# Kernel optimization log

Hardware: AMD Instinct MI355X
Metric: run time of the kernel (lower is better)

Reference implementation:

```python
import jax, jax.numpy as jnp
import numpy as np

B, S, D, H, DH = 2, 2048, 256, 8, 32
INNER = H * DH


def setup_inputs() -> dict:
    key = jax.random.key(0)
    ks = jax.random.split(key, 8)
    x = jax.random.normal(ks[0], (B, S, D), dtype=jnp.float32)
    mask = jax.random.randint(ks[1], (B, S), 0, 2) > 0  # bool, ~half valid
    attn_bias = jax.random.normal(ks[2], (B, H, S, S), dtype=jnp.float32) * 0.1
    Wq = jax.random.normal(ks[3], (D, INNER), dtype=jnp.float32) * 0.02
    Wkv = jax.random.normal(ks[4], (D, 2 * INNER), dtype=jnp.float32) * 0.02
    Wo = jax.random.normal(ks[5], (INNER, D), dtype=jnp.float32) * 0.02
    bo = jnp.zeros((D,), dtype=jnp.float32)
    Wg = jax.random.normal(ks[6], (D, INNER), dtype=jnp.float32) * 0.02
    bg = jnp.ones((INNER,), dtype=jnp.float32)  # torch init: gating bias = 1.0
    return {"x": x, "mask": mask, "attn_bias": attn_bias, "Wq": Wq,
            "Wkv": Wkv, "Wo": Wo, "bo": bo, "Wg": Wg, "bg": bg}


def reference(x, mask, attn_bias, Wq, Wkv, Wo, bo, Wg, bg):
    scale = DH ** -0.5
    b, s, _ = x.shape
    # q,k,v projections; '... i (h d) -> ... h i d'
    q = (x @ Wq).reshape(b, s, H, DH).swapaxes(1, 2)            # [b,h,s,d]
    kv = x @ Wkv
    k, v = jnp.split(kv, 2, axis=-1)
    k = k.reshape(b, s, H, DH).swapaxes(1, 2)                   # [b,h,s,d]
    v = v.reshape(b, s, H, DH).swapaxes(1, 2)                   # [b,h,s,d]
    # scores with additive bias and boolean masking
    dots = jnp.einsum('bhid,bhjd->bhij', q * scale, k) + attn_bias
    amask = mask[:, None, :, None] & mask[:, None, None, :]     # [b,1,i,j]
    neg = -jnp.finfo(dots.dtype).max
    dots = jnp.where(amask, dots, neg)
    attn = jax.nn.softmax(dots, axis=-1)                        # dropout p=0 (eval)
    out = jnp.einsum('bhij,bhjd->bhid', attn, v)
    out = out.swapaxes(1, 2).reshape(b, s, INNER)               # '... h i d -> ... i (h d)'
    gates = jax.nn.sigmoid(x @ Wg + bg)
    out = out * gates
    return out @ Wo + bo
```

## Files before the change

kernel.cpp:

```cpp
#include <hip/hip_runtime.h>
#include <float.h>

typedef unsigned short u16;
typedef __attribute__((ext_vector_type(8))) short bf16x8;
typedef __attribute__((ext_vector_type(4))) float f32x4;

#define LOG2E 1.4426950408889634f
#define B_ 2
#define S_ 2048
#define D_ 256
#define H_ 8
#define DH_ 32
#define M_ 4096

__device__ __forceinline__ void gload_lds16(const void* g, void* l) {
  __builtin_amdgcn_global_load_lds(
      (const __attribute__((address_space(1))) unsigned int*)g,
      (__attribute__((address_space(3))) unsigned int*)l, 16, 0, 0);
}

__device__ __forceinline__ u16 f2bf(float f) {
  unsigned u = __float_as_uint(f);
  unsigned r = (u + 0x7FFFu + ((u >> 16) & 1u)) >> 16;
  return (u16)r;
}

__global__ __launch_bounds__(256) void conv_x(const float* __restrict__ x,
                                              u16* __restrict__ xb) {
  int i = (blockIdx.x * 256 + threadIdx.x) * 4;
  float4 v = *(const float4*)(x + i);
  ushort4 o;
  o.x = f2bf(v.x); o.y = f2bf(v.y); o.z = f2bf(v.z); o.w = f2bf(v.w);
  *(ushort4*)(xb + i) = o;
}

__global__ __launch_bounds__(256) void prep_w(const float* __restrict__ Wq,
                                              const float* __restrict__ Wkv,
                                              const float* __restrict__ Wo,
                                              const float* __restrict__ Wg,
                                              u16* __restrict__ wt,
                                              u16* __restrict__ wot) {
  int t = blockIdx.x * 256 + threadIdx.x;
  const float scale = 0.17677669529663687f;
  if (t < 65536) {
    int k = t >> 8, n = t & 255;
    wt[(size_t)n * 256 + k] = f2bf(Wq[t] * scale);
  } else if (t < 196608) {
    int s = t - 65536;
    int k = s >> 9, c = s & 511;
    int n = (c < 256) ? (256 + c) : (512 + (c - 256));
    wt[(size_t)n * 256 + k] = f2bf(Wkv[s]);
  } else if (t < 262144) {
    int s = t - 196608;
    int k = s >> 8, n = s & 255;
    wt[(size_t)(768 + n) * 256 + k] = f2bf(Wg[s]);
  } else {
    int s = t - 262144;
    int k = s >> 8, n = s & 255;
    wot[(size_t)n * 256 + k] = f2bf(Wo[s]);
  }
}

__global__ __launch_bounds__(256) void gemm_proj(
    const u16* __restrict__ xb, const u16* __restrict__ wt,
    const float* __restrict__ bg, u16* __restrict__ qs, u16* __restrict__ kb,
    u16* __restrict__ vt, float* __restrict__ gates) {
  __shared__ u16 lA[128 * 32];
  __shared__ u16 lB[128 * 32];
  const int tid = threadIdx.x, l = tid & 63, w = tid >> 6;
  const int m0 = blockIdx.x * 128, n0 = blockIdx.y * 128;
  const int wm = w >> 1, wn = w & 1;
  f32x4 acc[4][4];
#pragma unroll
  for (int i = 0; i < 4; ++i)
#pragma unroll
    for (int j = 0; j < 4; ++j) acc[i][j] = (f32x4){0.f, 0.f, 0.f, 0.f};

  for (int ks = 0; ks < 8; ++ks) {
#pragma unroll
    for (int i = 0; i < 2; ++i) {
      int slot = i * 256 + tid;
      int row = slot >> 2, sk = slot & 3;
      int sw = sk ^ ((row >> 1) & 3);
      gload_lds16(xb + (size_t)(m0 + row) * 256 + ks * 32 + sw * 8,
                  (char*)lA + slot * 16);
    }
#pragma unroll
    for (int i = 0; i < 2; ++i) {
      int slot = i * 256 + tid;
      int row = slot >> 2, sk = slot & 3;
      int sw = sk ^ ((row >> 1) & 3);
      gload_lds16(wt + (size_t)(n0 + row) * 256 + ks * 32 + sw * 8,
                  (char*)lB + slot * 16);
    }
    __syncthreads();
    bf16x8 af[4], bfr[4];
#pragma unroll
    for (int mi = 0; mi < 4; ++mi) {
      int row = wm * 64 + mi * 16 + (l & 15);
      int koff = ((l >> 4) << 4) ^ (((row >> 1) & 3) << 4);
      af[mi] = *(const bf16x8*)((const char*)lA + row * 64 + koff);
    }
#pragma unroll
    for (int ni = 0; ni < 4; ++ni) {
      int row = wn * 64 + ni * 16 + (l & 15);
      int koff = ((l >> 4) << 4) ^ (((row >> 1) & 3) << 4);
      bfr[ni] = *(const bf16x8*)((const char*)lB + row * 64 + koff);
    }
#pragma unroll
    for (int mi = 0; mi < 4; ++mi)
#pragma unroll
      for (int ni = 0; ni < 4; ++ni)
        acc[mi][ni] = __builtin_amdgcn_mfma_f32_16x16x32_bf16(
            af[mi], bfr[ni], acc[mi][ni], 0, 0, 0);
    __syncthreads();
  }
  const int region = n0 >> 8;
#pragma unroll
  for (int mi = 0; mi < 4; ++mi)
#pragma unroll
    for (int ni = 0; ni < 4; ++ni) {
      int row = m0 + wm * 64 + mi * 16 + ((l >> 4) << 2);
      int col = n0 + wn * 64 + ni * 16 + (l & 15);
      int c = col & 255;
#pragma unroll
      for (int r = 0; r < 4; ++r) {
        float v = acc[mi][ni][r];
        int rr = row + r;
        int bq = rr >> 11, s = rr & 2047;
        if (region == 0) {
          int h = c >> 5, dh = c & 31;
          qs[((((size_t)bq * 8 + h) * 2048 + s) << 5) + dh] = f2bf(v);
        } else if (region == 1) {
          int h = c >> 5, dh = c & 31;
          kb[((((size_t)bq * 8 + h) * 2048 + s) << 5) + dh] = f2bf(v);
        } else if (region == 2) {
          int h = c >> 5, dh = c & 31;
          vt[((((size_t)bq * 8 + h) * 32 + dh) << 11) + s] = f2bf(v);
        } else {
          float g = 1.f / (1.f + expf(-(v + bg[c])));
          gates[(size_t)rr * 256 + c] = g;
        }
      }
    }
}

__global__ __launch_bounds__(256) void attn_fwd(
    const u16* __restrict__ qs, const u16* __restrict__ kb,
    const u16* __restrict__ vt, const float* __restrict__ bias,
    const int* __restrict__ mask, const float* __restrict__ gates,
    u16* __restrict__ ao) {
  __shared__ u16 lK[64 * 32];
  __shared__ u16 lV[32 * 64];
  __shared__ u16 lP[4][16 * 64];
  const int tid = threadIdx.x, l = tid & 63, w = tid >> 6;
  const int qt = blockIdx.x, h = blockIdx.y, b = blockIdx.z;
  const int q0 = qt * 64;
  const size_t bh = (size_t)b * H_ + h;

  const int qrow = q0 + w * 16 + (l & 15);
  bf16x8 qf = *(const bf16x8*)(qs + ((bh * S_ + qrow) << 5) + ((l >> 4) << 3));

  int rowr[4], mi_[4];
  float m_i[4], l_i[4];
  const float* biasrow[4];
  f32x4 acc_o[2];
  acc_o[0] = (f32x4){0.f, 0.f, 0.f, 0.f};
  acc_o[1] = (f32x4){0.f, 0.f, 0.f, 0.f};
#pragma unroll
  for (int r = 0; r < 4; ++r) {
    rowr[r] = q0 + w * 16 + ((l >> 4) << 2) + r;
    mi_[r] = mask[b * S_ + rowr[r]];
    m_i[r] = -FLT_MAX;
    l_i[r] = 0.f;
    biasrow[r] = bias + (bh * S_ + rowr[r]) * (size_t)S_;
  }

  for (int jc = 0; jc < 32; ++jc) {
    const int j0 = jc * 64;
    {
      int row = tid >> 2, sk = tid & 3;
      int sw = sk ^ ((row >> 1) & 3);
      gload_lds16(kb + ((bh * S_ + j0 + row) << 5) + sw * 8,
                  (char*)lK + tid * 16);
    }
    {
      int dh = tid >> 3, sk = tid & 7;
      int sw = sk ^ (dh & 7);
      gload_lds16(vt + ((bh * 32 + dh) << 11) + j0 + sw * 8,
                  (char*)lV + tid * 16);
    }
    __syncthreads();

    f32x4 sc[4];
#pragma unroll
    for (int cg = 0; cg < 4; ++cg) {
      int j = j0 + cg * 16 + (l & 15);
      int mj = mask[b * S_ + j];
      f32x4 ci;
#pragma unroll
      for (int r = 0; r < 4; ++r) {
        float bv = biasrow[r][j];
        ci[r] = (mi_[r] && mj) ? bv : -FLT_MAX;
      }
      int krow = cg * 16 + (l & 15);
      int koff = ((l >> 4) << 4) ^ (((krow >> 1) & 3) << 4);
      bf16x8 kf = *(const bf16x8*)((const char*)lK + krow * 64 + koff);
      sc[cg] = __builtin_amdgcn_mfma_f32_16x16x32_bf16(qf, kf, ci, 0, 0, 0);
    }

    float corr[4];
#pragma unroll
    for (int r = 0; r < 4; ++r) {
      float v0 = fmaxf(fmaxf(sc[0][r], sc[1][r]), fmaxf(sc[2][r], sc[3][r]));
#pragma unroll
      for (int off = 1; off < 16; off <<= 1) v0 = fmaxf(v0, __shfl_xor(v0, off));
      float mn = fmaxf(m_i[r], v0);
      corr[r] = exp2f((m_i[r] - mn) * LOG2E);
      m_i[r] = mn;
    }
    float rs[4] = {0.f, 0.f, 0.f, 0.f};
#pragma unroll
    for (int cg = 0; cg < 4; ++cg) {
#pragma unroll
      for (int r = 0; r < 4; ++r) {
        float p = exp2f((sc[cg][r] - m_i[r]) * LOG2E);
        rs[r] += p;
        int prow = ((l >> 4) << 2) + r;
        int col = cg * 16 + (l & 15);
        *(u16*)((char*)lP[w] + prow * 128 + ((col * 2) ^ ((prow & 7) << 4))) =
            f2bf(p);
      }
    }
#pragma unroll
    for (int r = 0; r < 4; ++r) {
      float s = rs[r];
#pragma unroll
      for (int off = 1; off < 16; off <<= 1) s += __shfl_xor(s, off);
      l_i[r] = l_i[r] * corr[r] + s;
    }
#pragma unroll
    for (int g = 0; g < 2; ++g)
#pragma unroll
      for (int r = 0; r < 4; ++r) acc_o[g][r] *= corr[r];

#pragma unroll
    for (int kp = 0; kp < 2; ++kp) {
      int prow = l & 15;
      int koff = (((l >> 4) << 4) + kp * 64) ^ ((prow & 7) << 4);
      bf16x8 pf = *(const bf16x8*)((const char*)lP[w] + prow * 128 + koff);
#pragma unroll
      for (int g = 0; g < 2; ++g) {
        int vrow = g * 16 + (l & 15);
        int vkoff = (((l >> 4) << 4) + kp * 64) ^ ((vrow & 7) << 4);
        bf16x8 vf = *(const bf16x8*)((const char*)lV + vrow * 128 + vkoff);
        acc_o[g] = __builtin_amdgcn_mfma_f32_16x16x32_bf16(pf, vf, acc_o[g], 0, 0, 0);
      }
    }
    __syncthreads();
  }

#pragma unroll
  for (int g = 0; g < 2; ++g)
#pragma unroll
    for (int r = 0; r < 4; ++r) {
      int rr = rowr[r];
      int dh = g * 16 + (l & 15);
      float gate = gates[(size_t)(b * S_ + rr) * 256 + h * 32 + dh];
      float o = acc_o[g][r] / l_i[r] * gate;
      ao[(size_t)(b * S_ + rr) * 256 + h * 32 + dh] = f2bf(o);
    }
}

__global__ __launch_bounds__(256) void gemm_out(const u16* __restrict__ ao,
                                                const u16* __restrict__ wot,
                                                const float* __restrict__ bo,
                                                float* __restrict__ out) {
  __shared__ u16 lA[128 * 32];
  __shared__ u16 lB[128 * 32];
  const int tid = threadIdx.x, l = tid & 63, w = tid >> 6;
  const int m0 = blockIdx.x * 128, n0 = blockIdx.y * 128;
  const int wm = w >> 1, wn = w & 1;
  f32x4 acc[4][4];
#pragma unroll
  for (int i = 0; i < 4; ++i)
#pragma unroll
    for (int j = 0; j < 4; ++j) acc[i][j] = (f32x4){0.f, 0.f, 0.f, 0.f};

  for (int ks = 0; ks < 8; ++ks) {
#pragma unroll
    for (int i = 0; i < 2; ++i) {
      int slot = i * 256 + tid;
      int row = slot >> 2, sk = slot & 3;
      int sw = sk ^ ((row >> 1) & 3);
      gload_lds16(ao + (size_t)(m0 + row) * 256 + ks * 32 + sw * 8,
                  (char*)lA + slot * 16);
    }
#pragma unroll
    for (int i = 0; i < 2; ++i) {
      int slot = i * 256 + tid;
      int row = slot >> 2, sk = slot & 3;
      int sw = sk ^ ((row >> 1) & 3);
      gload_lds16(wot + (size_t)(n0 + row) * 256 + ks * 32 + sw * 8,
                  (char*)lB + slot * 16);
    }
    __syncthreads();
    bf16x8 af[4], bfr[4];
#pragma unroll
    for (int mi = 0; mi < 4; ++mi) {
      int row = wm * 64 + mi * 16 + (l & 15);
      int koff = ((l >> 4) << 4) ^ (((row >> 1) & 3) << 4);
      af[mi] = *(const bf16x8*)((const char*)lA + row * 64 + koff);
    }
#pragma unroll
    for (int ni = 0; ni < 4; ++ni) {
      int row = wn * 64 + ni * 16 + (l & 15);
      int koff = ((l >> 4) << 4) ^ (((row >> 1) & 3) << 4);
      bfr[ni] = *(const bf16x8*)((const char*)lB + row * 64 + koff);
    }
#pragma unroll
    for (int mi = 0; mi < 4; ++mi)
#pragma unroll
      for (int ni = 0; ni < 4; ++ni)
        acc[mi][ni] = __builtin_amdgcn_mfma_f32_16x16x32_bf16(
            af[mi], bfr[ni], acc[mi][ni], 0, 0, 0);
    __syncthreads();
  }
#pragma unroll
  for (int mi = 0; mi < 4; ++mi)
#pragma unroll
    for (int ni = 0; ni < 4; ++ni) {
      int row = m0 + wm * 64 + mi * 16 + ((l >> 4) << 2);
      int col = n0 + wn * 64 + ni * 16 + (l & 15);
#pragma unroll
      for (int r = 0; r < 4; ++r)
        out[(size_t)(row + r) * 256 + col] = acc[mi][ni][r] + bo[col];
    }
}

extern "C" void kernel_launch(void* const* d_in, const int* in_sizes, int n_in,
                              void* d_out, int out_size, void* d_ws,
                              size_t ws_size, hipStream_t stream) {
  const float* x   = (const float*)d_in[0];
  const int* mask  = (const int*)d_in[1];
  const float* bias = (const float*)d_in[2];
  const float* Wq  = (const float*)d_in[3];
  const float* Wkv = (const float*)d_in[4];
  const float* Wo  = (const float*)d_in[5];
  const float* bo  = (const float*)d_in[6];
  const float* Wg  = (const float*)d_in[7];
  const float* bg  = (const float*)d_in[8];

  char* ws = (char*)d_ws;
  u16* xb      = (u16*)(ws);
  u16* wt      = (u16*)(ws + 2097152);
  u16* wot     = (u16*)(ws + 2621440);
  u16* qs      = (u16*)(ws + 2752512);
  u16* kb      = (u16*)(ws + 4849664);
  u16* vt      = (u16*)(ws + 6946816);
  float* gates = (float*)(ws + 9043968);
  u16* ao      = (u16*)(ws + 13238272);
  float* out   = (float*)d_out;

  conv_x<<<dim3(1024), dim3(256), 0, stream>>>(x, xb);
  prep_w<<<dim3(1280), dim3(256), 0, stream>>>(Wq, Wkv, Wo, Wg, wt, wot);
  gemm_proj<<<dim3(32, 8), dim3(256), 0, stream>>>(xb, wt, bg, qs, kb, vt, gates);
  attn_fwd<<<dim3(32, 8, 2), dim3(256), 0, stream>>>(qs, kb, vt, bias, mask, gates, ao);
  gemm_out<<<dim3(32, 2), dim3(256), 0, stream>>>(ao, wot, bo, out);
}
```

Measured before the change: 430.4 us.

## Double-buffer K/V/bias tiles in attention and projection GEMM; bit-pack key mask

Both gemm_proj and attn_fwd now use double-buffered LDS with async global-to-LDS loads of the next tile issued before computing the current one, synchronised with explicit vmcnt waits and barriers. In attention, the attn_bias tile is also staged through LDS instead of being read as scattered global loads per lane. The key mask is precomputed into per-column bitmasks by a new tiny kernel, so each iteration uses a register shift instead of a global load. This costs more LDS (32KB bias buffers), which may reduce occupancy, plus an extra kernel launch.

```diff
diff --git a/kernel.cpp b/kernel.cpp
--- a/kernel.cpp
+++ b/kernel.cpp
@@ -61,12 +61,22 @@
   }
 }
 
+__global__ __launch_bounds__(64) void pack_mask(const int* __restrict__ mask,
+                                                unsigned* __restrict__ cmT) {
+  int b = blockIdx.x, c = threadIdx.x;
+  unsigned wd = 0;
+#pragma unroll
+  for (int jc = 0; jc < 32; ++jc)
+    wd |= (unsigned)(mask[b * 2048 + jc * 64 + c] & 1) << jc;
+  cmT[b * 64 + c] = wd;
+}
+
 __global__ __launch_bounds__(256) void gemm_proj(
     const u16* __restrict__ xb, const u16* __restrict__ wt,
     const float* __restrict__ bg, u16* __restrict__ qs, u16* __restrict__ kb,
     u16* __restrict__ vt, float* __restrict__ gates) {
-  __shared__ u16 lA[128 * 32];
-  __shared__ u16 lB[128 * 32];
+  __shared__ u16 lA[2][128 * 32];
+  __shared__ u16 lB[2][128 * 32];
   const int tid = threadIdx.x, l = tid & 63, w = tid >> 6;
   const int m0 = blockIdx.x * 128, n0 = blockIdx.y * 128;
   const int wm = w >> 1, wn = w & 1;
@@ -76,14 +86,14 @@
 #pragma unroll
     for (int j = 0; j < 4; ++j) acc[i][j] = (f32x4){0.f, 0.f, 0.f, 0.f};
 
-  for (int ks = 0; ks < 8; ++ks) {
+  auto stage = [&](int ks, int p) {
 #pragma unroll
     for (int i = 0; i < 2; ++i) {
       int slot = i * 256 + tid;
       int row = slot >> 2, sk = slot & 3;
       int sw = sk ^ ((row >> 1) & 3);
       gload_lds16(xb + (size_t)(m0 + row) * 256 + ks * 32 + sw * 8,
-                  (char*)lA + slot * 16);
+                  (char*)lA[p] + slot * 16);
     }
 #pragma unroll
     for (int i = 0; i < 2; ++i) {
@@ -91,21 +101,36 @@
       int row = slot >> 2, sk = slot & 3;
       int sw = sk ^ ((row >> 1) & 3);
       gload_lds16(wt + (size_t)(n0 + row) * 256 + ks * 32 + sw * 8,
-                  (char*)lB + slot * 16);
-    }
-    __syncthreads();
+                  (char*)lB[p] + slot * 16);
+    }
+  };
+
+  stage(0, 0);
+  asm volatile("s_waitcnt vmcnt(0)" ::: "memory");
+  __builtin_amdgcn_s_barrier();
+
+  for (int ks = 0; ks < 8; ++ks) {
+    const int cur = ks & 1;
+    if (ks < 7) {
+      stage(ks + 1, cur ^ 1);
+      asm volatile("s_waitcnt vmcnt(4)" ::: "memory");
+    } else {
+      asm volatile("s_waitcnt vmcnt(0)" ::: "memory");
+    }
+    __builtin_amdgcn_s_barrier();
+
     bf16x8 af[4], bfr[4];
 #pragma unroll
     for (int mi = 0; mi < 4; ++mi) {
       int row = wm * 64 + mi * 16 + (l & 15);
       int koff = ((l >> 4) << 4) ^ (((row >> 1) & 3) << 4);
-      af[mi] = *(const bf16x8*)((const char*)lA + row * 64 + koff);
+      af[mi] = *(const bf16x8*)((const char*)lA[cur] + row * 64 + koff);
     }
 #pragma unroll
     for (int ni = 0; ni < 4; ++ni) {
       int row = wn * 64 + ni * 16 + (l & 15);
       int koff = ((l >> 4) << 4) ^ (((row >> 1) & 3) << 4);
-      bfr[ni] = *(const bf16x8*)((const char*)lB + row * 64 + koff);
+      bfr[ni] = *(const bf16x8*)((const char*)lB[cur] + row * 64 + koff);
     }
 #pragma unroll
     for (int mi = 0; mi < 4; ++mi)
@@ -113,7 +138,8 @@
       for (int ni = 0; ni < 4; ++ni)
         acc[mi][ni] = __builtin_amdgcn_mfma_f32_16x16x32_bf16(
             af[mi], bfr[ni], acc[mi][ni], 0, 0, 0);
-    __syncthreads();
+    __builtin_amdgcn_sched_barrier(0);
+    __builtin_amdgcn_s_barrier();
   }
   const int region = n0 >> 8;
 #pragma unroll
@@ -148,10 +174,11 @@
 __global__ __launch_bounds__(256) void attn_fwd(
     const u16* __restrict__ qs, const u16* __restrict__ kb,
     const u16* __restrict__ vt, const float* __restrict__ bias,
-    const int* __restrict__ mask, const float* __restrict__ gates,
-    u16* __restrict__ ao) {
-  __shared__ u16 lK[64 * 32];
-  __shared__ u16 lV[32 * 64];
+    const int* __restrict__ mask, const unsigned* __restrict__ cmT,
+    const float* __restrict__ gates, u16* __restrict__ ao) {
+  __shared__ u16 lK[2][64 * 32];
+  __shared__ u16 lV[2][32 * 64];
+  __shared__ float lBias[2][64 * 64];
   __shared__ u16 lP[4][16 * 64];
   const int tid = threadIdx.x, l = tid & 63, w = tid >> 6;
   const int qt = blockIdx.x, h = blockIdx.y, b = blockIdx.z;
@@ -163,49 +190,72 @@
 
   int rowr[4], mi_[4];
   float m_i[4], l_i[4];
-  const float* biasrow[4];
+  unsigned cm[4];
   f32x4 acc_o[2];
   acc_o[0] = (f32x4){0.f, 0.f, 0.f, 0.f};
   acc_o[1] = (f32x4){0.f, 0.f, 0.f, 0.f};
 #pragma unroll
   for (int r = 0; r < 4; ++r) {
     rowr[r] = q0 + w * 16 + ((l >> 4) << 2) + r;
-    mi_[r] = mask[b * S_ + rowr[r]];
+    mi_[r] = mask[b * S_ + rowr[r]] & 1;
     m_i[r] = -FLT_MAX;
     l_i[r] = 0.f;
-    biasrow[r] = bias + (bh * S_ + rowr[r]) * (size_t)S_;
   }
-
-  for (int jc = 0; jc < 32; ++jc) {
+#pragma unroll
+  for (int cg = 0; cg < 4; ++cg) cm[cg] = cmT[(b << 6) + cg * 16 + (l & 15)];
+
+  auto stage = [&](int jc, int p) {
     const int j0 = jc * 64;
     {
       int row = tid >> 2, sk = tid & 3;
       int sw = sk ^ ((row >> 1) & 3);
       gload_lds16(kb + ((bh * S_ + j0 + row) << 5) + sw * 8,
-                  (char*)lK + tid * 16);
+                  (char*)lK[p] + tid * 16);
     }
     {
       int dh = tid >> 3, sk = tid & 7;
       int sw = sk ^ (dh & 7);
       gload_lds16(vt + ((bh * 32 + dh) << 11) + j0 + sw * 8,
-                  (char*)lV + tid * 16);
-    }
-    __syncthreads();
+                  (char*)lV[p] + tid * 16);
+    }
+#pragma unroll
+    for (int i = 0; i < 4; ++i) {
+      int u = i * 256 + tid;
+      int row = u >> 4, cb = u & 15;
+      gload_lds16(bias + (bh * S_ + q0 + row) * (size_t)S_ + j0 + cb * 4,
+                  (char*)lBias[p] + u * 16);
+    }
+  };
+
+  stage(0, 0);
+  asm volatile("s_waitcnt vmcnt(0)" ::: "memory");
+  __builtin_amdgcn_s_barrier();
+
+  for (int jc = 0; jc < 32; ++jc) {
+    const int cur = jc & 1;
+    if (jc < 31) {
+      stage(jc + 1, cur ^ 1);
+      asm volatile("s_waitcnt vmcnt(6)" ::: "memory");
+    } else {
+      asm volatile("s_waitcnt vmcnt(0)" ::: "memory");
+    }
+    __builtin_amdgcn_s_barrier();
 
     f32x4 sc[4];
 #pragma unroll
     for (int cg = 0; cg < 4; ++cg) {
-      int j = j0 + cg * 16 + (l & 15);
-      int mj = mask[b * S_ + j];
+      int colj = cg * 16 + (l & 15);
+      int mj = (int)((cm[cg] >> jc) & 1u);
       f32x4 ci;
 #pragma unroll
       for (int r = 0; r < 4; ++r) {
-        float bv = biasrow[r][j];
-        ci[r] = (mi_[r] && mj) ? bv : -FLT_MAX;
+        int qlr = w * 16 + ((l >> 4) << 2) + r;
+        float bv = lBias[cur][qlr * 64 + colj];
+        ci[r] = (mi_[r] & mj) ? bv : -FLT_MAX;
       }
       int krow = cg * 16 + (l & 15);
       int koff = ((l >> 4) << 4) ^ (((krow >> 1) & 3) << 4);
-      bf16x8 kf = *(const bf16x8*)((const char*)lK + krow * 64 + koff);
+      bf16x8 kf = *(const bf16x8*)((const char*)lK[cur] + krow * 64 + koff);
       sc[cg] = __builtin_amdgcn_mfma_f32_16x16x32_bf16(qf, kf, ci, 0, 0, 0);
     }
 
@@ -253,11 +303,12 @@
       for (int g = 0; g < 2; ++g) {
         int vrow = g * 16 + (l & 15);
         int vkoff = (((l >> 4) << 4) + kp * 64) ^ ((vrow & 7) << 4);
-        bf16x8 vf = *(const bf16x8*)((const char*)lV + vrow * 128 + vkoff);
+        bf16x8 vf = *(const bf16x8*)((const char*)lV[cur] + vrow * 128 + vkoff);
         acc_o[g] = __builtin_amdgcn_mfma_f32_16x16x32_bf16(pf, vf, acc_o[g], 0, 0, 0);
       }
     }
-    __syncthreads();
+    __builtin_amdgcn_sched_barrier(0);
+    __builtin_amdgcn_s_barrier();
   }
 
 #pragma unroll
@@ -360,11 +411,13 @@
   u16* vt      = (u16*)(ws + 6946816);
   float* gates = (float*)(ws + 9043968);
   u16* ao      = (u16*)(ws + 13238272);
+  unsigned* cmT = (unsigned*)(ws + 15335424);
   float* out   = (float*)d_out;
 
   conv_x<<<dim3(1024), dim3(256), 0, stream>>>(x, xb);
   prep_w<<<dim3(1280), dim3(256), 0, stream>>>(Wq, Wkv, Wo, Wg, wt, wot);
+  pack_mask<<<dim3(2), dim3(64), 0, stream>>>(mask, cmT);
   gemm_proj<<<dim3(32, 8), dim3(256), 0, stream>>>(xb, wt, bg, qs, kb, vt, gates);
-  attn_fwd<<<dim3(32, 8, 2), dim3(256), 0, stream>>>(qs, kb, vt, bias, mask, gates, ao);
+  attn_fwd<<<dim3(32, 8, 2), dim3(256), 0, stream>>>(qs, kb, vt, bias, mask, cmT, gates, ao);
   gemm_out<<<dim3(32, 2), dim3(256), 0, stream>>>(ao, wot, bo, out);
 }
```

Measured after the change: 438.6 us. Within noise of the previous version (+1.9%).
